# Kernel optimization log

Hardware: AMD Instinct MI355X
Metric: run time of the kernel (lower is better)

The kernel has to match this reference:

```python
import jax, jax.numpy as jnp
import numpy as np
import math

B, S, SENC, D, H, FF, V = 4, 512, 512, 1024, 16, 4096, 50257
MAX_HOP = 6          # n_layers -> max ACT hops
THRESH = 1.0 - 0.01  # ACT halting threshold
EPS = 1e-12          # LAYER_NORM_EPS
NEG = -1e20          # neginf for fp32 masking
DH = D // H


def _sincos(n_pos, dim):
    # create_position_codes: sin on even dims, cos on odd dims
    pos = np.arange(n_pos, dtype=np.float64)[:, None]
    j = np.arange(dim // 2, dtype=np.float64)[None, :]
    ang = pos / np.power(10000.0, 2.0 * j / dim)
    out = np.zeros((n_pos, dim), dtype=np.float32)
    out[:, 0::2] = np.sin(ang)
    out[:, 1::2] = np.cos(ang)
    return jnp.asarray(out)


def setup_inputs() -> dict:
    key = jax.random.key(0)
    ks = jax.random.split(key, 20)
    def lin_w(k, fan_in, fan_out):
        return (jax.random.normal(k, (fan_in, fan_out), jnp.float32)
                * (1.0 / math.sqrt(fan_in)))
    inp = {
        "tokens": jax.random.randint(ks[0], (B, S), 0, V),
        "encoder_output": jax.random.normal(ks[1], (B, SENC, D), jnp.float32),
        "encoder_mask": jnp.ones((B, SENC), jnp.int32),
        "emb": jax.random.normal(ks[2], (V, D), jnp.float32) * 0.02,
        "sa_qw": lin_w(ks[3], D, D), "sa_qb": jnp.zeros((D,), jnp.float32),
        "sa_kw": lin_w(ks[4], D, D), "sa_kb": jnp.zeros((D,), jnp.float32),
        "sa_vw": lin_w(ks[5], D, D), "sa_vb": jnp.zeros((D,), jnp.float32),
        "sa_ow": lin_w(ks[6], D, D), "sa_ob": jnp.zeros((D,), jnp.float32),
        "ca_qw": lin_w(ks[7], D, D), "ca_qb": jnp.zeros((D,), jnp.float32),
        "ca_kw": lin_w(ks[8], D, D), "ca_kb": jnp.zeros((D,), jnp.float32),
        "ca_vw": lin_w(ks[9], D, D), "ca_vb": jnp.zeros((D,), jnp.float32),
        "ca_ow": lin_w(ks[10], D, D), "ca_ob": jnp.zeros((D,), jnp.float32),
        "ln1_g": jnp.ones((D,), jnp.float32), "ln1_b": jnp.zeros((D,), jnp.float32),
        "ln2_g": jnp.ones((D,), jnp.float32), "ln2_b": jnp.zeros((D,), jnp.float32),
        "ln3_g": jnp.ones((D,), jnp.float32), "ln3_b": jnp.zeros((D,), jnp.float32),
        "ff_w1": lin_w(ks[11], D, FF), "ff_b1": jnp.zeros((FF,), jnp.float32),
        "ff_w2": lin_w(ks[12], FF, D), "ff_b2": jnp.zeros((D,), jnp.float32),
        "act_w": jax.random.normal(ks[13], (D,), jnp.float32) * 0.02,
        "act_b": jnp.ones((), jnp.float32),  # p.bias.data.fill_(1)
    }
    return inp


def _ln(x, g, b):
    m = x.mean(-1, keepdims=True)
    v = ((x - m) ** 2).mean(-1, keepdims=True)
    return (x - m) / jnp.sqrt(v + EPS) * g + b


def _mha(x, kv, maskb, qw, qb, kw, kb, vw, vb, ow, ob):
    Bq, Sq, _ = x.shape
    Sk = kv.shape[1]
    q = (x @ qw + qb).reshape(Bq, Sq, H, DH).transpose(0, 2, 1, 3) / math.sqrt(DH)
    k = (kv @ kw + kb).reshape(Bq, Sk, H, DH).transpose(0, 2, 1, 3)
    v = (kv @ vw + vb).reshape(Bq, Sk, H, DH).transpose(0, 2, 1, 3)
    sc = jnp.einsum('bhqd,bhkd->bhqk', q, k)
    sc = jnp.where(maskb, sc, NEG)
    a = jax.nn.softmax(sc, axis=-1)
    o = jnp.einsum('bhqk,bhkd->bhqd', a, v).transpose(0, 2, 1, 3).reshape(Bq, Sq, D)
    return o @ ow + ob


def reference(tokens, encoder_output, encoder_mask, emb,
              sa_qw, sa_qb, sa_kw, sa_kb, sa_vw, sa_vb, sa_ow, sa_ob,
              ca_qw, ca_qb, ca_kw, ca_kb, ca_vw, ca_vb, ca_ow, ca_ob,
              ln1_g, ln1_b, ln2_g, ln2_b, ln3_g, ln3_b,
              ff_w1, ff_b1, ff_w2, ff_b2, act_w, act_b):
    pos_codes = _sincos(S, D)       # [S, D]
    time_codes = _sincos(MAX_HOP, D)  # [MAX_HOP, D]
    x = emb[tokens] * math.sqrt(D)  # embeddings_scale
    dec_mask = jnp.tril(jnp.ones((S, S), bool))[None, None]          # causal
    enc_maskb = (encoder_mask != 0)[:, None, None, :]                # [B,1,1,Senc]

    def layer(t):
        r = t
        t = _mha(t, t, dec_mask, sa_qw, sa_qb, sa_kw, sa_kb, sa_vw, sa_vb, sa_ow, sa_ob)
        t = _ln(t + r, ln1_g, ln1_b)
        r = t
        t = _mha(t, encoder_output, enc_maskb, ca_qw, ca_qb, ca_kw, ca_kb, ca_vw, ca_vb, ca_ow, ca_ob)
        t = _ln(t + r, ln2_g, ln2_b)
        r = t
        t = jax.nn.relu(t @ ff_w1 + ff_b1) @ ff_w2 + ff_b2
        return _ln(t + r, ln3_g, ln3_b)

    def step(carry, t_idx):
        tensor, prev, hp, rem, nup = carry
        tensor = tensor + pos_codes[None] + time_codes[t_idx][None, None]
        p = jax.nn.sigmoid(tensor @ act_w + act_b)                   # [B,S]
        still = (hp < 1.0).astype(jnp.float32)
        cond = hp + p * still
        new_halted = (cond > THRESH).astype(jnp.float32) * still
        still = (cond <= THRESH).astype(jnp.float32) * still
        hp = hp + p * still
        rem = rem + new_halted * (1.0 - hp)
        hp = hp + new_halted * rem
        nup = nup + still + new_halted
        uw = (p * still + new_halted * rem)[..., None]
        tensor = layer(tensor)
        prev = tensor * uw + prev * (1.0 - uw)
        return (tensor, prev, hp, rem, nup), None

    z = jnp.zeros((B, S), jnp.float32)
    init = (x, jnp.zeros_like(x), z, z, z)
    # Running all MAX_HOP steps is exactly equivalent to the torch while-loop:
    # after a position halts, its update weight is 0 and state is frozen.
    (_, prev, hp, rem, nup), _ = jax.lax.scan(step, init, jnp.arange(MAX_HOP))
    return prev
```

## Files before the change

### kernel.cpp

```cpp
#include <hip/hip_runtime.h>
#include <math.h>

#define BB 4
#define SS 512
#define SE 512
#define DD 1024
#define HH 16
#define FFD 4096
#define NHOP 6

typedef float f32x4 __attribute__((ext_vector_type(4)));
typedef _Float16 h8 __attribute__((ext_vector_type(8)));
typedef _Float16 h4 __attribute__((ext_vector_type(4)));

#define GLD16(gp, lp)                                                     \
  __builtin_amdgcn_global_load_lds(                                       \
      (const __attribute__((address_space(1))) void*)(gp),                \
      (__attribute__((address_space(3))) void*)(lp), 16, 0, 0)

template <int N>
__device__ __forceinline__ void vwait() {
  if constexpr (N == 0) asm volatile("s_waitcnt vmcnt(0)" ::: "memory");
  else if constexpr (N == 6) asm volatile("s_waitcnt vmcnt(6)" ::: "memory");
  else if constexpr (N == 8) asm volatile("s_waitcnt vmcnt(8)" ::: "memory");
}

__device__ __forceinline__ float blockSum256(float v, float* s4) {
#pragma unroll
  for (int m = 32; m >= 1; m >>= 1) v += __shfl_xor(v, m);
  __syncthreads();
  if ((threadIdx.x & 63) == 0) s4[threadIdx.x >> 6] = v;
  __syncthreads();
  return s4[0] + s4[1] + s4[2] + s4[3];
}

__device__ __forceinline__ void split16(float v, _Float16& h, _Float16& l) {
  h = (_Float16)v;
  l = (_Float16)(v - (float)h);
}

__device__ __forceinline__ int swzel(int row, int slot) {
  return (row << 6) + ((slot ^ (row & 7)) << 3);
}

__global__ void sincos_kernel(float* __restrict__ out, int n) {
  for (int i = blockIdx.x * blockDim.x + threadIdx.x; i < n;
       i += gridDim.x * blockDim.x) {
    int p = i >> 10, d = i & 1023, j = d >> 1;
    double ang = (double)p / pow(10000.0, (2.0 * j) / 1024.0);
    out[i] = (float)((d & 1) ? cos(ang) : sin(ang));
  }
}

__global__ void embed_kernel(const int* __restrict__ tok,
                             const float* __restrict__ emb,
                             float* __restrict__ out, int n) {
  for (int i = blockIdx.x * blockDim.x + threadIdx.x; i < n;
       i += gridDim.x * blockDim.x) {
    int row = i >> 10, d = i & 1023;
    out[i] = emb[(size_t)tok[row] * DD + d] * 32.0f;
  }
}

__global__ void asplit_kernel(const float* __restrict__ x,
                              _Float16* __restrict__ h,
                              _Float16* __restrict__ l, int n) {
  for (int i = blockIdx.x * blockDim.x + threadIdx.x; i < n;
       i += gridDim.x * blockDim.x)
    split16(x[i], h[i], l[i]);
}

__global__ __launch_bounds__(256)
void actcodes_kernel(const float* __restrict__ ten, const float* __restrict__ pos,
                     const float* __restrict__ tim, int hop,
                     const float* __restrict__ aw, const float* __restrict__ ab,
                     float* __restrict__ hp, float* __restrict__ rem,
                     float* __restrict__ uw, _Float16* __restrict__ th,
                     _Float16* __restrict__ tl) {
  __shared__ float s4[4];
  int row = blockIdx.x;
  int srow = row & 511;
  size_t base = (size_t)row * DD;
  float s = 0.f;
#pragma unroll
  for (int k = 0; k < 4; ++k) {
    int d = threadIdx.x + k * 256;
    float v = ten[base + d] + pos[(srow << 10) + d] + tim[(hop << 10) + d];
    split16(v, th[base + d], tl[base + d]);
    s += v * aw[d];
  }
  float z = blockSum256(s, s4);
  if (threadIdx.x == 0) {
    z += ab[0];
    float p = 1.0f / (1.0f + expf(-z));
    float h = hp[row], rm = rem[row];
    float s0 = (h < 1.0f) ? 1.0f : 0.0f;
    float cond = h + p * s0;
    float nh = (cond > 0.99f) ? s0 : 0.0f;
    float s1 = (cond <= 0.99f) ? s0 : 0.0f;
    h = h + p * s1;
    rm = rm + nh * (1.0f - h);
    h = h + nh * rm;
    hp[row] = h;
    rem[row] = rm;
    uw[row] = p * s1 + nh * rm;
  }
}

__global__ __launch_bounds__(256)
void lnres_kernel(const float* __restrict__ a, const _Float16* __restrict__ rh,
                  const _Float16* __restrict__ rl, const float* __restrict__ g,
                  const float* __restrict__ be, float* __restrict__ outf,
                  _Float16* __restrict__ oh, _Float16* __restrict__ ol,
                  const float* __restrict__ uwv, float* __restrict__ po,
                  int mode) {
  __shared__ float s4[4];
  int row = blockIdx.x;
  size_t base = (size_t)row * DD;
  float x[4];
#pragma unroll
  for (int k = 0; k < 4; ++k) {
    size_t idx = base + threadIdx.x + k * 256;
    x[k] = a[idx] + ((float)rh[idx] + (float)rl[idx]);
  }
  float mean = blockSum256(x[0] + x[1] + x[2] + x[3], s4) * (1.0f / 1024.0f);
  float q = 0.f;
#pragma unroll
  for (int k = 0; k < 4; ++k) {
    float dv = x[k] - mean;
    q += dv * dv;
  }
  float var = blockSum256(q, s4) * (1.0f / 1024.0f);
  float inv = 1.0f / sqrtf(var + 1e-12f);
  float u = (mode == 0) ? uwv[row] : 0.f;
#pragma unroll
  for (int k = 0; k < 4; ++k) {
    int d = threadIdx.x + k * 256;
    size_t idx = base + d;
    float y = (x[k] - mean) * inv * g[d] + be[d];
    if (mode == 0) {
      outf[idx] = y;
      po[idx] = y * u + po[idx] * (1.0f - u);
    } else {
      split16(y, oh[idx], ol[idx]);
    }
  }
}

__global__ __launch_bounds__(256)
void wsplit_kernel(const float* __restrict__ W, _Float16* __restrict__ WhT,
                   _Float16* __restrict__ WlT, int K, int N) {
  __shared__ float t[32][33];
  int k0 = blockIdx.y << 5, n0 = blockIdx.x << 5;
  int c = threadIdx.x & 31, r8 = threadIdx.x >> 5;
  for (int rr = r8; rr < 32; rr += 8)
    t[rr][c] = W[(size_t)(k0 + rr) * N + n0 + c];
  __syncthreads();
  for (int rr = r8; rr < 32; rr += 8) {
    float v = t[c][rr];
    split16(v, WhT[(size_t)(n0 + rr) * K + k0 + c],
            WlT[(size_t)(n0 + rr) * K + k0 + c]);
  }
}

__global__ void concat3_kernel(const float* __restrict__ a,
                               const float* __restrict__ b,
                               const float* __restrict__ c,
                               float* __restrict__ o) {
  int i = blockIdx.x * 256 + threadIdx.x;
  if (i < 3072) o[i] = (i < 1024) ? a[i] : ((i < 2048) ? b[i - 1024] : c[i - 2048]);
}

template <int EPI>
__global__ __launch_bounds__(256) void gemm_pl(
    const _Float16* __restrict__ Ah, const _Float16* __restrict__ Al,
    const _Float16* __restrict__ Bh, const _Float16* __restrict__ Bl,
    const float* __restrict__ bias, float* __restrict__ Cf,
    _Float16* __restrict__ Ch, _Float16* __restrict__ Cl,
    _Float16* __restrict__ Ch2, _Float16* __restrict__ Cl2,
    _Float16* __restrict__ Ch3, _Float16* __restrict__ Cl3, int M, int N,
    int K, float scale) {
  __shared__ __align__(16) _Float16 sA0[2][4096], sA1[2][4096];
  __shared__ __align__(16) _Float16 sB0[2][4096], sB1[2][4096];
  const int tid = threadIdx.x;
  const int lane = tid & 63, wid = tid >> 6;
  const int wr = wid >> 1, wc = wid & 1;
  int bx = blockIdx.x, by = blockIdx.y;
  {
    int nb = gridDim.x * gridDim.y;
    if ((nb & 7) == 0) {
      int flat = by * gridDim.x + bx;
      int swz = (flat & 7) * (nb >> 3) + (flat >> 3);
      bx = swz % gridDim.x;
      by = swz / gridDim.x;
    }
  }
  const int m0 = by << 6, n0 = bx << 6;
  const int l15 = lane & 15, l4 = lane >> 4;

  f32x4 acc[2][2];
#pragma unroll
  for (int i = 0; i < 2; ++i)
#pragma unroll
    for (int j = 0; j < 2; ++j) acc[i][j] = (f32x4){0.f, 0.f, 0.f, 0.f};

  auto STAGE = [&](int kt, int buf) {
    const int ko = kt << 6;
#pragma unroll
    for (int c = 0; c < 2; ++c) {
      int idx = (c << 8) + tid;
      int row = idx >> 3, gs = (idx & 7) ^ (row & 7);
      int de = (c << 11) + (wid << 9);
      size_t ga = (size_t)(m0 + row) * K + ko + (gs << 3);
      GLD16(Ah + ga, &sA0[buf][de]);
      GLD16(Al + ga, &sA1[buf][de]);
      size_t gb = (size_t)(n0 + row) * K + ko + (gs << 3);
      GLD16(Bh + gb, &sB0[buf][de]);
      GLD16(Bl + gb, &sB1[buf][de]);
    }
  };

  const int nk = K >> 6;
  STAGE(0, 0);
  int cur = 0;
  for (int kt = 0; kt < nk; ++kt) {
    if (kt + 1 < nk) {
      STAGE(kt + 1, cur ^ 1);
      vwait<8>();
    } else {
      vwait<0>();
    }
    __builtin_amdgcn_s_barrier();
    __builtin_amdgcn_sched_barrier(0);
    const _Float16* pA0 = sA0[cur];
    const _Float16* pA1 = sA1[cur];
    const _Float16* pB0 = sB0[cur];
    const _Float16* pB1 = sB1[cur];
#pragma unroll
    for (int ks = 0; ks < 2; ++ks) {
      h8 a0[2], a1[2], b0[2], b1[2];
#pragma unroll
      for (int f = 0; f < 2; ++f) {
        int m = (wr << 5) + (f << 4) + l15;
        int so = swzel(m, (ks << 2) + l4);
        a0[f] = *(const h8*)&pA0[so];
        a1[f] = *(const h8*)&pA1[so];
        int n = (wc << 5) + (f << 4) + l15;
        int sn = swzel(n, (ks << 2) + l4);
        b0[f] = *(const h8*)&pB0[sn];
        b1[f] = *(const h8*)&pB1[sn];
      }
#pragma unroll
      for (int fi = 0; fi < 2; ++fi)
#pragma unroll
        for (int fj = 0; fj < 2; ++fj) {
          acc[fi][fj] = __builtin_amdgcn_mfma_f32_16x16x32_f16(
              a0[fi], b0[fj], acc[fi][fj], 0, 0, 0);
          acc[fi][fj] = __builtin_amdgcn_mfma_f32_16x16x32_f16(
              a1[fi], b0[fj], acc[fi][fj], 0, 0, 0);
          acc[fi][fj] = __builtin_amdgcn_mfma_f32_16x16x32_f16(
              a0[fi], b1[fj], acc[fi][fj], 0, 0, 0);
        }
    }
    __builtin_amdgcn_sched_barrier(0);
    __builtin_amdgcn_s_barrier();
    cur ^= 1;
  }
#pragma unroll
  for (int fi = 0; fi < 2; ++fi) {
    int row = m0 + (wr << 5) + (fi << 4) + (l4 << 2);
#pragma unroll
    for (int fj = 0; fj < 2; ++fj) {
      int col = n0 + (wc << 5) + (fj << 4) + l15;
      float bz = bias[col];
      float ov[4];
#pragma unroll
      for (int r = 0; r < 4; ++r) ov[r] = acc[fi][fj][r] + bz;
      if (EPI == 0) {
#pragma unroll
        for (int r = 0; r < 4; ++r) Cf[(size_t)(row + r) * N + col] = ov[r];
      } else if (EPI == 1) {
#pragma unroll
        for (int r = 0; r < 4; ++r) {
          float o = fmaxf(ov[r], 0.f);
          size_t idx = (size_t)(row + r) * N + col;
          split16(o, Ch[idx], Cl[idx]);
        }
      } else if (EPI == 3) {
        int b = row >> 9, h = col >> 6, d = col & 63;
#pragma unroll
        for (int r = 0; r < 4; ++r) {
          int sr = (row + r) & 511;
          size_t q = ((size_t)(b * HH + h) * SS + sr) * 64 + d;
          split16(ov[r] * scale, Ch[q], Cl[q]);
        }
      } else if (EPI == 4) {
        int b = row >> 9, s0 = row & 511, h = col >> 6, d = col & 63;
        h4 hv, lv;
#pragma unroll
        for (int r = 0; r < 4; ++r) {
          _Float16 hh, ll;
          split16(ov[r], hh, ll);
          hv[r] = hh;
          lv[r] = ll;
        }
        size_t vo = ((size_t)(b * HH + h) * 64 + d) * SS + s0;
        *(h4*)&Ch[vo] = hv;
        *(h4*)&Cl[vo] = lv;
      }
    }
  }
}

template <int EPI>
__global__ __launch_bounds__(256) void gemm_big(
    const _Float16* __restrict__ Ah, const _Float16* __restrict__ Al,
    const _Float16* __restrict__ Bh, const _Float16* __restrict__ Bl,
    const float* __restrict__ bias, _Float16* __restrict__ Ch,
    _Float16* __restrict__ Cl, _Float16* __restrict__ Ch2,
    _Float16* __restrict__ Cl2, _Float16* __restrict__ Ch3,
    _Float16* __restrict__ Cl3, int M, int N, int K, float scale) {
  constexpr int FM = 4, FN = 2;
  constexpr int MT = 128, NT = 64;
  constexpr int SA = 2, SB = 1;
  constexpr int L = 2 * (SA + SB);
  __shared__ __align__(16) _Float16 sA0[2][MT * 32], sA1[2][MT * 32];
  __shared__ __align__(16) _Float16 sB0[2][NT * 32], sB1[2][NT * 32];
  const int tid = threadIdx.x;
  const int lane = tid & 63, wid = tid >> 6;
  const int wr = wid >> 1, wc = wid & 1;
  int bx = blockIdx.x, by = blockIdx.y;
  {
    int nb = gridDim.x * gridDim.y;
    if ((nb & 7) == 0) {
      int flat = by * gridDim.x + bx;
      int swz = (flat & 7) * (nb >> 3) + (flat >> 3);
      bx = swz % gridDim.x;
      by = swz / gridDim.x;
    }
  }
  const int m0 = by * MT, n0 = bx * NT;
  const int l15 = lane & 15, l4 = lane >> 4;

  f32x4 acc[FM][FN];
#pragma unroll
  for (int i = 0; i < FM; ++i)
#pragma unroll
    for (int j = 0; j < FN; ++j) acc[i][j] = (f32x4){0.f, 0.f, 0.f, 0.f};

  auto STAGE = [&](int kt, int buf) {
    const int ko = kt << 5;
#pragma unroll
    for (int c = 0; c < SA; ++c) {
      int slot = tid + (c << 8);
      int row = slot >> 2, sl = slot & 3;
      int of = ((sl ^ ((row >> 1) & 3)) << 3);
      size_t ga = (size_t)(m0 + row) * K + ko + of;
      int de = (wid << 9) + (c << 11);
      GLD16(Ah + ga, &sA0[buf][de]);
      GLD16(Al + ga, &sA1[buf][de]);
    }
#pragma unroll
    for (int c = 0; c < SB; ++c) {
      int slot = tid + (c << 8);
      int row = slot >> 2, sl = slot & 3;
      int of = ((sl ^ ((row >> 1) & 3)) << 3);
      size_t gb = (size_t)(n0 + row) * K + ko + of;
      int de = (wid << 9) + (c << 11);
      GLD16(Bh + gb, &sB0[buf][de]);
      GLD16(Bl + gb, &sB1[buf][de]);
    }
  };

  const int nk = K >> 5;
  STAGE(0, 0);
  int cur = 0;
  for (int kt = 0; kt < nk; ++kt) {
    if (kt + 1 < nk) {
      STAGE(kt + 1, cur ^ 1);
      vwait<L>();
    } else {
      vwait<0>();
    }
    __builtin_amdgcn_s_barrier();
    __builtin_amdgcn_sched_barrier(0);
    const _Float16* pA0 = sA0[cur];
    const _Float16* pA1 = sA1[cur];
    const _Float16* pB0 = sB0[cur];
    const _Float16* pB1 = sB1[cur];
    h8 a0[FM], a1[FM], b0[FN], b1[FN];
#pragma unroll
    for (int f = 0; f < FM; ++f) {
      int m = wr * (FM * 16) + f * 16 + l15;
      int st = ((l4 ^ ((m >> 1) & 3)) << 3);
      a0[f] = *(const h8*)&pA0[(m << 5) + st];
      a1[f] = *(const h8*)&pA1[(m << 5) + st];
    }
#pragma unroll
    for (int f = 0; f < FN; ++f) {
      int n = wc * (FN * 16) + f * 16 + l15;
      int sn = ((l4 ^ ((n >> 1) & 3)) << 3);
      b0[f] = *(const h8*)&pB0[(n << 5) + sn];
      b1[f] = *(const h8*)&pB1[(n << 5) + sn];
    }
#pragma unroll
    for (int fi = 0; fi < FM; ++fi)
#pragma unroll
      for (int fj = 0; fj < FN; ++fj) {
        acc[fi][fj] = __builtin_amdgcn_mfma_f32_16x16x32_f16(
            a0[fi], b0[fj], acc[fi][fj], 0, 0, 0);
        acc[fi][fj] = __builtin_amdgcn_mfma_f32_16x16x32_f16(
            a1[fi], b0[fj], acc[fi][fj], 0, 0, 0);
        acc[fi][fj] = __builtin_amdgcn_mfma_f32_16x16x32_f16(
            a0[fi], b1[fj], acc[fi][fj], 0, 0, 0);
      }
    __builtin_amdgcn_sched_barrier(0);
    __builtin_amdgcn_s_barrier();
    cur ^= 1;
  }
#pragma unroll
  for (int fi = 0; fi < FM; ++fi) {
    int row = m0 + wr * (FM * 16) + fi * 16 + (l4 << 2);
#pragma unroll
    for (int fj = 0; fj < FN; ++fj) {
      int col = n0 + wc * (FN * 16) + fj * 16 + l15;
      float bz = bias[col];
      float ov[4];
#pragma unroll
      for (int r = 0; r < 4; ++r) ov[r] = acc[fi][fj][r] + bz;
      if (EPI == 1) {
#pragma unroll
        for (int r = 0; r < 4; ++r) {
          float o = fmaxf(ov[r], 0.f);
          size_t idx = (size_t)(row + r) * N + col;
          split16(o, Ch[idx], Cl[idx]);
        }
      } else {
        int reg = col >> 10;
        int c = col & 1023;
        int b = row >> 9, h = c >> 6, d = c & 63;
        if (reg == 2) {
          int s0 = row & 511;
          h4 hv, lv;
#pragma unroll
          for (int r = 0; r < 4; ++r) {
            _Float16 hh, ll;
            split16(ov[r], hh, ll);
            hv[r] = hh;
            lv[r] = ll;
          }
          size_t vo = ((size_t)(b * HH + h) * 64 + d) * SS + s0;
          *(h4*)&Ch3[vo] = hv;
          *(h4*)&Cl3[vo] = lv;
        } else {
#pragma unroll
          for (int r = 0; r < 4; ++r) {
            float o = (reg == 0) ? ov[r] * scale : ov[r];
            int sr = (row + r) & 511;
            size_t q = ((size_t)(b * HH + h) * SS + sr) * 64 + d;
            if (reg == 0) split16(o, Ch[q], Cl[q]);
            else split16(o, Ch2[q], Cl2[q]);
          }
        }
      }
    }
  }
}

template <int CAUSAL>
__global__ __launch_bounds__(256) void flash_mfma(
    const _Float16* __restrict__ Qph, const _Float16* __restrict__ Qpl,
    const _Float16* __restrict__ Kph, const _Float16* __restrict__ Kpl,
    const _Float16* __restrict__ Vph, const _Float16* __restrict__ Vpl,
    _Float16* __restrict__ AOh, _Float16* __restrict__ AOl,
    const int* __restrict__ mask, int Sk) {
  __shared__ __align__(16) _Float16 sKh[2][4096], sKl[2][4096];
  __shared__ __align__(16) _Float16 sVh[2][4096], sVl[2][4096];
  __shared__ __align__(16) _Float16 sPh[4096], sPl[4096];
  const int tid = threadIdx.x, lane = tid & 63, wid = tid >> 6;
  const int l15 = lane & 15, l4 = lane >> 4;
  const int flat = blockIdx.x;
  const int bh = flat >> 3, b = bh >> 4;
  int qt = flat & 7;
  if (CAUSAL && (flat >> 8)) qt = 7 - qt;
  const size_t qkb = (size_t)bh * SS * 64;
  const size_t vtb = (size_t)bh * 64 * Sk;

  int srow[2], slg[2], sde[2];
#pragma unroll
  for (int c = 0; c < 2; ++c) {
    int u = (c << 8) + tid;
    srow[c] = u >> 3;
    slg[c] = (u & 7) ^ (srow[c] & 7);
    sde[c] = (c << 11) + (wid << 9);
  }

  unsigned mbits = 0xFFFFFFFFu;
  if (!CAUSAL && mask != nullptr) {
    mbits = 0u;
#pragma unroll
    for (int kt = 0; kt < 8; ++kt)
#pragma unroll
      for (int fj = 0; fj < 4; ++fj)
        mbits |= (mask[b * Sk + kt * 64 + fj * 16 + l15] != 0 ? 1u : 0u)
                 << (kt * 4 + fj);
  }

  h8 aqh[2], aql[2];
#pragma unroll
  for (int ks = 0; ks < 2; ++ks) {
    size_t qa = qkb + (size_t)(qt * 64 + wid * 16 + l15) * 64 + ks * 32 + l4 * 8;
    aqh[ks] = *(const h8*)(Qph + qa);
    aql[ks] = *(const h8*)(Qpl + qa);
  }
  f32x4 o_[4];
  float m_[4], l_[4];
#pragma unroll
  for (int i = 0; i < 4; ++i) o_[i] = (f32x4){0.f, 0.f, 0.f, 0.f};
#pragma unroll
  for (int r = 0; r < 4; ++r) { m_[r] = -3.0e38f; l_[r] = 0.f; }

  auto STAGE = [&](int kt, int buf) {
#pragma unroll
    for (int c = 0; c < 2; ++c) {
      size_t ksrc = qkb + (size_t)(kt * 64 + srow[c]) * 64 + slg[c] * 8;
      size_t vsrc = vtb + (size_t)srow[c] * Sk + kt * 64 + slg[c] * 8;
      GLD16(Kph + ksrc, &sKh[buf][sde[c]]);
      GLD16(Kpl + ksrc, &sKl[buf][sde[c]]);
      GLD16(Vph + vsrc, &sVh[buf][sde[c]]);
      GLD16(Vpl + vsrc, &sVl[buf][sde[c]]);
    }
  };

  const int nkt = CAUSAL ? (qt + 1) : (Sk >> 6);
  STAGE(0, 0);
  int cur = 0;
  for (int kt = 0; kt < nkt; ++kt) {
    if (kt + 1 < nkt) {
      STAGE(kt + 1, cur ^ 1);
      vwait<8>();
    } else {
      vwait<0>();
    }
    __builtin_amdgcn_s_barrier();
    __builtin_amdgcn_sched_barrier(0);
    const _Float16* pKh = sKh[cur];
    const _Float16* pKl = sKl[cur];
    const _Float16* pVh = sVh[cur];
    const _Float16* pVl = sVl[cur];
    f32x4 sc[4];
#pragma unroll
    for (int fj = 0; fj < 4; ++fj) {
      sc[fj] = (f32x4){0.f, 0.f, 0.f, 0.f};
#pragma unroll
      for (int ks = 0; ks < 2; ++ks) {
        int off = swzel(fj * 16 + l15, ks * 4 + l4);
        h8 bkh = *(const h8*)&pKh[off];
        h8 bkl = *(const h8*)&pKl[off];
        sc[fj] = __builtin_amdgcn_mfma_f32_16x16x32_f16(aqh[ks], bkh, sc[fj], 0, 0, 0);
        sc[fj] = __builtin_amdgcn_mfma_f32_16x16x32_f16(aql[ks], bkh, sc[fj], 0, 0, 0);
        sc[fj] = __builtin_amdgcn_mfma_f32_16x16x32_f16(aqh[ks], bkl, sc[fj], 0, 0, 0);
      }
    }
    if (CAUSAL && kt == qt) {
#pragma unroll
      for (int fj = 0; fj < 4; ++fj)
#pragma unroll
        for (int r = 0; r < 4; ++r)
          if (fj * 16 + l15 > wid * 16 + l4 * 4 + r) sc[fj][r] = -1e20f;
    }
    if (!CAUSAL) {
#pragma unroll
      for (int fj = 0; fj < 4; ++fj)
        if (!((mbits >> (kt * 4 + fj)) & 1u)) {
#pragma unroll
          for (int r = 0; r < 4; ++r) sc[fj][r] = -1e20f;
        }
    }
#pragma unroll
    for (int r = 0; r < 4; ++r) {
      float rm = fmaxf(fmaxf(sc[0][r], sc[1][r]), fmaxf(sc[2][r], sc[3][r]));
#pragma unroll
      for (int mk = 1; mk < 16; mk <<= 1) rm = fmaxf(rm, __shfl_xor(rm, mk));
      float mn = fmaxf(m_[r], rm);
      float f = __expf(m_[r] - mn);
      float rs = 0.f;
      int prow = wid * 16 + l4 * 4 + r;
#pragma unroll
      for (int fj = 0; fj < 4; ++fj) {
        float p = __expf(sc[fj][r] - mn);
        rs += p;
        int col = fj * 16 + l15;
        int el = (prow << 6) + ((((col >> 3) ^ (prow & 7))) << 3) + (col & 7);
        _Float16 ph = (_Float16)p;
        sPh[el] = ph;
        sPl[el] = (_Float16)(p - (float)ph);
      }
#pragma unroll
      for (int mk = 1; mk < 16; mk <<= 1) rs += __shfl_xor(rs, mk);
      l_[r] = l_[r] * f + rs;
      m_[r] = mn;
#pragma unroll
      for (int df = 0; df < 4; ++df) o_[df][r] *= f;
    }
#pragma unroll
    for (int ks = 0; ks < 2; ++ks) {
      int poff = swzel(wid * 16 + l15, ks * 4 + l4);
      h8 aph = *(const h8*)&sPh[poff];
      h8 apl = *(const h8*)&sPl[poff];
#pragma unroll
      for (int df = 0; df < 4; ++df) {
        int voff = swzel(df * 16 + l15, ks * 4 + l4);
        h8 bvh = *(const h8*)&pVh[voff];
        h8 bvl = *(const h8*)&pVl[voff];
        o_[df] = __builtin_amdgcn_mfma_f32_16x16x32_f16(aph, bvh, o_[df], 0, 0, 0);
        o_[df] = __builtin_amdgcn_mfma_f32_16x16x32_f16(apl, bvh, o_[df], 0, 0, 0);
        o_[df] = __builtin_amdgcn_mfma_f32_16x16x32_f16(aph, bvl, o_[df], 0, 0, 0);
      }
    }
    __builtin_amdgcn_sched_barrier(0);
    __builtin_amdgcn_s_barrier();
    cur ^= 1;
  }
#pragma unroll
  for (int r = 0; r < 4; ++r) {
    float inv = 1.0f / l_[r];
    int row = qt * 64 + wid * 16 + l4 * 4 + r;
    size_t ob = ((size_t)b * SS + row) * DD + (bh & 15) * 64;
#pragma unroll
    for (int df = 0; df < 4; ++df) {
      float o = o_[df][r] * inv;
      split16(o, AOh[ob + df * 16 + l15], AOl[ob + df * 16 + l15]);
    }
  }
}

extern "C" void kernel_launch(void* const* d_in, const int* in_sizes, int n_in,
                              void* d_out, int out_size, void* d_ws,
                              size_t ws_size, hipStream_t stream) {
  const int* tokens = (const int*)d_in[0];
  const float* enc = (const float*)d_in[1];
  const int* encmask = (const int*)d_in[2];
  const float* emb = (const float*)d_in[3];
  const float* sa_qw = (const float*)d_in[4];
  const float* sa_qb = (const float*)d_in[5];
  const float* sa_kw = (const float*)d_in[6];
  const float* sa_kb = (const float*)d_in[7];
  const float* sa_vw = (const float*)d_in[8];
  const float* sa_vb = (const float*)d_in[9];
  const float* sa_ow = (const float*)d_in[10];
  const float* sa_ob = (const float*)d_in[11];
  const float* ca_qw = (const float*)d_in[12];
  const float* ca_qb = (const float*)d_in[13];
  const float* ca_kw = (const float*)d_in[14];
  const float* ca_kb = (const float*)d_in[15];
  const float* ca_vw = (const float*)d_in[16];
  const float* ca_vb = (const float*)d_in[17];
  const float* ca_ow = (const float*)d_in[18];
  const float* ca_ob = (const float*)d_in[19];
  const float* ln1_g = (const float*)d_in[20];
  const float* ln1_b = (const float*)d_in[21];
  const float* ln2_g = (const float*)d_in[22];
  const float* ln2_b = (const float*)d_in[23];
  const float* ln3_g = (const float*)d_in[24];
  const float* ln3_b = (const float*)d_in[25];
  const float* ff_w1 = (const float*)d_in[26];
  const float* ff_b1 = (const float*)d_in[27];
  const float* ff_w2 = (const float*)d_in[28];
  const float* ff_b2 = (const float*)d_in[29];
  const float* act_w = (const float*)d_in[30];
  const float* act_b = (const float*)d_in[31];
  float* out = (float*)d_out;

  const size_t nbsd = (size_t)BB * SS * DD;
  const size_t nff = (size_t)BB * SS * FFD;
  const size_t nbs = (size_t)BB * SS;
  const size_t wsm = (size_t)DD * DD;
  const size_t wff = (size_t)DD * FFD;

  float* w = (float*)d_ws;
  float* POS = w;  w += (size_t)SS * DD;
  float* TIM = w;  w += (size_t)NHOP * DD;
  float* TEN = w;  w += nbsd;
  float* PR = w;   w += nbsd;
  float* T2R = w;  w += (size_t)2048 * 3072;
  float* QKVB = w; w += 3072;
  float* HPp = w;  w += nbs;
  float* REMp = w; w += nbs;
  float* UWp = w;  w += nbs;
  _Float16* hp16 = (_Float16*)w;
  auto halloc = [&](size_t n) { _Float16* r = hp16; hp16 += n; return r; };
  _Float16* TINh = halloc(nbsd); _Float16* TINl = halloc(nbsd);
  _Float16* AOh = halloc(nbsd);  _Float16* AOl = halloc(nbsd);
  _Float16* FFHh = halloc(nff);  _Float16* FFHl = halloc(nff);
  _Float16* qkvWh = halloc(3 * wsm); _Float16* qkvWl = halloc(3 * wsm);
  _Float16* saoWh = halloc(wsm); _Float16* saoWl = halloc(wsm);
  _Float16* caqWh = halloc(wsm); _Float16* caqWl = halloc(wsm);
  _Float16* caoWh = halloc(wsm); _Float16* caoWl = halloc(wsm);
  _Float16* ff1Wh = halloc(wff); _Float16* ff1Wl = halloc(wff);
  _Float16* ff2Wh = halloc(wff); _Float16* ff2Wl = halloc(wff);
  _Float16* EKh = halloc(nbsd); _Float16* EKl = halloc(nbsd);
  _Float16* EVh = halloc(nbsd); _Float16* EVl = halloc(nbsd);
  size_t need = (size_t)((char*)hp16 - (char*)d_ws);
  if (ws_size < need) return;

  _Float16* T3h = TINh; _Float16* T3l = TINl;
  _Float16* T2h = (_Float16*)T2R;
  _Float16* T2l = (_Float16*)T2R + nbsd;
  _Float16* Qph = FFHh;             _Float16* Qpl = FFHh + nbsd;
  _Float16* Kph = FFHh + 2 * nbsd;  _Float16* Kpl = FFHh + 3 * nbsd;
  _Float16* Vph = FFHl;             _Float16* Vpl = FFHl + nbsd;
  _Float16* CQh = FFHl + 2 * nbsd;  _Float16* CQl = FFHl + 3 * nbsd;

  hipMemsetAsync(d_out, 0, nbsd * sizeof(float), stream);
  hipMemsetAsync(HPp, 0, 2 * nbs * sizeof(float), stream);
  sincos_kernel<<<dim3(512), dim3(256), 0, stream>>>(POS, SS * DD);
  sincos_kernel<<<dim3(24), dim3(256), 0, stream>>>(TIM, NHOP * DD);
  embed_kernel<<<dim3(2048), dim3(256), 0, stream>>>(tokens, emb, TEN, (int)nbsd);
  asplit_kernel<<<dim3(2048), dim3(256), 0, stream>>>(enc, TINh, TINl, (int)nbsd);

  auto wsplit = [&](const float* W, _Float16* h, _Float16* l, int K, int N) {
    wsplit_kernel<<<dim3(N >> 5, K >> 5), dim3(256), 0, stream>>>(W, h, l, K, N);
  };
  wsplit(sa_qw, qkvWh, qkvWl, DD, DD);
  wsplit(sa_kw, qkvWh + wsm, qkvWl + wsm, DD, DD);
  wsplit(sa_vw, qkvWh + 2 * wsm, qkvWl + 2 * wsm, DD, DD);
  wsplit(sa_ow, saoWh, saoWl, DD, DD);
  wsplit(ca_qw, caqWh, caqWl, DD, DD);
  wsplit(ca_kw, FFHh, FFHh + wsm, DD, DD);
  wsplit(ca_vw, FFHh + 2 * wsm, FFHh + 3 * wsm, DD, DD);
  wsplit(ca_ow, caoWh, caoWl, DD, DD);
  wsplit(ff_w1, ff1Wh, ff1Wl, DD, FFD);
  wsplit(ff_w2, ff2Wh, ff2Wl, FFD, DD);
  concat3_kernel<<<dim3(12), dim3(256), 0, stream>>>(sa_qb, sa_kb, sa_vb, QKVB);

  auto gemmF = [&](const _Float16* ah, const _Float16* al, const _Float16* bh,
                   const _Float16* bl, const float* bi, float* cf, int M, int N,
                   int K) {
    gemm_pl<0><<<dim3(N / 64, M / 64), dim3(256), 0, stream>>>(
        ah, al, bh, bl, bi, cf, nullptr, nullptr, nullptr, nullptr, nullptr,
        nullptr, M, N, K, 1.f);
  };

  gemm_pl<3><<<dim3(16, 32), dim3(256), 0, stream>>>(
      TINh, TINl, FFHh, FFHh + wsm, ca_kb, nullptr, EKh, EKl, nullptr, nullptr,
      nullptr, nullptr, 2048, DD, DD, 1.f);
  gemm_pl<4><<<dim3(16, 32), dim3(256), 0, stream>>>(
      TINh, TINl, FFHh + 2 * wsm, FFHh + 3 * wsm, ca_vb, nullptr, EVh, EVl,
      nullptr, nullptr, nullptr, nullptr, 2048, DD, DD, 1.f);

  for (int t = 0; t < NHOP; ++t) {
    actcodes_kernel<<<dim3(2048), dim3(256), 0, stream>>>(
        TEN, POS, TIM, t, act_w, act_b, HPp, REMp, UWp, TINh, TINl);
    gemm_big<2><<<dim3(48, 16), dim3(256), 0, stream>>>(
        TINh, TINl, qkvWh, qkvWl, QKVB, Qph, Qpl, Kph, Kpl, Vph, Vpl, 2048,
        3072, DD, 0.125f);
    flash_mfma<1><<<dim3(512), dim3(256), 0, stream>>>(
        Qph, Qpl, Kph, Kpl, Vph, Vpl, AOh, AOl, nullptr, SS);
    gemmF(AOh, AOl, saoWh, saoWl, sa_ob, PR, 2048, DD, DD);
    lnres_kernel<<<dim3(2048), dim3(256), 0, stream>>>(
        PR, TINh, TINl, ln1_g, ln1_b, nullptr, T2h, T2l, nullptr, nullptr, 1);
    gemm_pl<3><<<dim3(16, 32), dim3(256), 0, stream>>>(
        T2h, T2l, caqWh, caqWl, ca_qb, nullptr, CQh, CQl, nullptr, nullptr,
        nullptr, nullptr, 2048, DD, DD, 0.125f);
    flash_mfma<0><<<dim3(512), dim3(256), 0, stream>>>(
        CQh, CQl, EKh, EKl, EVh, EVl, AOh, AOl, encmask, SE);
    gemmF(AOh, AOl, caoWh, caoWl, ca_ob, PR, 2048, DD, DD);
    lnres_kernel<<<dim3(2048), dim3(256), 0, stream>>>(
        PR, T2h, T2l, ln2_g, ln2_b, nullptr, T3h, T3l, nullptr, nullptr, 1);
    gemm_big<1><<<dim3(64, 16), dim3(256), 0, stream>>>(
        T3h, T3l, ff1Wh, ff1Wl, ff_b1, FFHh, FFHl, nullptr, nullptr, nullptr,
        nullptr, 2048, FFD, DD, 1.f);
    gemmF(FFHh, FFHl, ff2Wh, ff2Wl, ff_b2, PR, 2048, DD, FFD);
    lnres_kernel<<<dim3(2048), dim3(256), 0, stream>>>(
        PR, T3h, T3l, ln3_g, ln3_b, TEN, nullptr, nullptr, UWp, out, 0);
  }
}
```

Before: 2.059 ms.

## Load GEMM B fragments straight into registers, bypassing LDS

The split-fp16 GEMM no longer stages the B operand (high and low halves) through shared memory. Each wave now loads its B fragments directly from global memory into registers, double-buffered across a K loop unrolled by two. The vmcnt waits are widened to cover the extra in-flight loads. This halves LDS footprint and cuts LDS read traffic, which may help occupancy. The cost is that waves sharing a column tile fetch the same B data twice from cache, registers holding B fragments go up, and the unrolled loop assumes an even number of K tiles.

```diff
diff --git a/kernel.cpp b/kernel.cpp
--- a/kernel.cpp
+++ b/kernel.cpp
@@ -23,6 +23,7 @@
   if constexpr (N == 0) asm volatile("s_waitcnt vmcnt(0)" ::: "memory");
   else if constexpr (N == 6) asm volatile("s_waitcnt vmcnt(6)" ::: "memory");
   else if constexpr (N == 8) asm volatile("s_waitcnt vmcnt(8)" ::: "memory");
+  else if constexpr (N == 12) asm volatile("s_waitcnt vmcnt(12)" ::: "memory");
 }
 
 __device__ __forceinline__ float blockSum256(float v, float* s4) {
@@ -181,7 +182,6 @@
     _Float16* __restrict__ Ch3, _Float16* __restrict__ Cl3, int M, int N,
     int K, float scale) {
   __shared__ __align__(16) _Float16 sA0[2][4096], sA1[2][4096];
-  __shared__ __align__(16) _Float16 sB0[2][4096], sB1[2][4096];
   const int tid = threadIdx.x;
   const int lane = tid & 63, wid = tid >> 6;
   const int wr = wid >> 1, wc = wid & 1;
@@ -214,54 +214,71 @@
       size_t ga = (size_t)(m0 + row) * K + ko + (gs << 3);
       GLD16(Ah + ga, &sA0[buf][de]);
       GLD16(Al + ga, &sA1[buf][de]);
-      size_t gb = (size_t)(n0 + row) * K + ko + (gs << 3);
-      GLD16(Bh + gb, &sB0[buf][de]);
-      GLD16(Bl + gb, &sB1[buf][de]);
     }
   };
-
-  const int nk = K >> 6;
-  STAGE(0, 0);
-  int cur = 0;
-  for (int kt = 0; kt < nk; ++kt) {
-    if (kt + 1 < nk) {
-      STAGE(kt + 1, cur ^ 1);
-      vwait<8>();
-    } else {
-      vwait<0>();
-    }
-    __builtin_amdgcn_s_barrier();
-    __builtin_amdgcn_sched_barrier(0);
-    const _Float16* pA0 = sA0[cur];
-    const _Float16* pA1 = sA1[cur];
-    const _Float16* pB0 = sB0[cur];
-    const _Float16* pB1 = sB1[cur];
+  auto BLOAD = [&](int kt, h8 (&c0)[2][2], h8 (&c1)[2][2]) {
+#pragma unroll
+    for (int f = 0; f < 2; ++f)
+#pragma unroll
+      for (int ks = 0; ks < 2; ++ks) {
+        int n = (wc << 5) + (f << 4) + l15;
+        size_t gb = (size_t)(n0 + n) * K + (kt << 6) + (ks << 5) + (l4 << 3);
+        c0[f][ks] = *(const h8*)(Bh + gb);
+        c1[f][ks] = *(const h8*)(Bl + gb);
+      }
+  };
+  auto COMPUTE = [&](int buf, h8 (&c0)[2][2], h8 (&c1)[2][2]) {
+    const _Float16* pA0 = sA0[buf];
+    const _Float16* pA1 = sA1[buf];
 #pragma unroll
     for (int ks = 0; ks < 2; ++ks) {
-      h8 a0[2], a1[2], b0[2], b1[2];
+      h8 a0[2], a1[2];
 #pragma unroll
       for (int f = 0; f < 2; ++f) {
         int m = (wr << 5) + (f << 4) + l15;
         int so = swzel(m, (ks << 2) + l4);
         a0[f] = *(const h8*)&pA0[so];
         a1[f] = *(const h8*)&pA1[so];
-        int n = (wc << 5) + (f << 4) + l15;
-        int sn = swzel(n, (ks << 2) + l4);
-        b0[f] = *(const h8*)&pB0[sn];
-        b1[f] = *(const h8*)&pB1[sn];
       }
 #pragma unroll
       for (int fi = 0; fi < 2; ++fi)
 #pragma unroll
         for (int fj = 0; fj < 2; ++fj) {
           acc[fi][fj] = __builtin_amdgcn_mfma_f32_16x16x32_f16(
-              a0[fi], b0[fj], acc[fi][fj], 0, 0, 0);
+              a0[fi], c0[fj][ks], acc[fi][fj], 0, 0, 0);
           acc[fi][fj] = __builtin_amdgcn_mfma_f32_16x16x32_f16(
-              a1[fi], b0[fj], acc[fi][fj], 0, 0, 0);
+              a1[fi], c0[fj][ks], acc[fi][fj], 0, 0, 0);
           acc[fi][fj] = __builtin_amdgcn_mfma_f32_16x16x32_f16(
-              a0[fi], b1[fj], acc[fi][fj], 0, 0, 0);
+              a0[fi], c1[fj][ks], acc[fi][fj], 0, 0, 0);
         }
     }
+  };
+
+  h8 e0[2][2], e1[2][2], o0[2][2], o1[2][2];
+  const int nk = K >> 6;
+  STAGE(0, 0);
+  BLOAD(0, e0, e1);
+  int cur = 0;
+  for (int kt = 0; kt + 1 < nk; kt += 2) {
+    STAGE(kt + 1, cur ^ 1);
+    BLOAD(kt + 1, o0, o1);
+    vwait<12>();
+    __builtin_amdgcn_s_barrier();
+    __builtin_amdgcn_sched_barrier(0);
+    COMPUTE(cur, e0, e1);
+    __builtin_amdgcn_sched_barrier(0);
+    __builtin_amdgcn_s_barrier();
+    cur ^= 1;
+    if (kt + 2 < nk) {
+      STAGE(kt + 2, cur ^ 1);
+      BLOAD(kt + 2, e0, e1);
+      vwait<12>();
+    } else {
+      vwait<0>();
+    }
+    __builtin_amdgcn_s_barrier();
+    __builtin_amdgcn_sched_barrier(0);
+    COMPUTE(cur, o0, o1);
     __builtin_amdgcn_sched_barrier(0);
     __builtin_amdgcn_s_barrier();
     cur ^= 1;
```

Measured after the change: 2.829 ms. 37.4% more time.
